# Optimization experiments

Measured on AMD Instinct MI355X. Metric: run time of the kernel, lower is better.

Reference implementation:

```python
import jax, jax.numpy as jnp
import numpy as np

B, N, F, H = 2, 2048, 1024, 16
HD = F // H
SQRT_D = float(np.sqrt(F))  # note: module scales by sqrt(in_c), not sqrt(head_dim)


def setup_inputs() -> dict:
    key = jax.random.key(0)
    ks = jax.random.split(key, 9)
    s = 1.0 / np.sqrt(F)
    mk = lambda k: jax.random.uniform(k, (F, F), jnp.float32, -s, s)
    mb = lambda k: jax.random.uniform(k, (F,), jnp.float32, -s, s)
    return {
        "x": jax.random.normal(ks[0], (B, N, F), jnp.float32),
        "Wq": mk(ks[1]), "bq": mb(ks[2]),
        "Wk": mk(ks[3]), "bk": mb(ks[4]),
        "Wv": mk(ks[5]), "bv": mb(ks[6]),
        "Wo": mk(ks[7]), "bo": mb(ks[8]),
    }


def reference(x, Wq, bq, Wk, bk, Wv, bv, Wo, bo):
    b, n, f = x.shape
    # projections (torch Linear: x @ W.T + b); view to (b, n, h, hd)
    q = (x @ Wq.T + bq).reshape(b, n, H, HD)
    k = (x @ Wk.T + bk).reshape(b, n, H, HD)
    v = (x @ Wv.T + bv).reshape(b, n, H, HD)
    score = jnp.einsum('bihd,bjhd->bhij', q, k)
    attn = jax.nn.softmax(score / SQRT_D, axis=-1)
    o = jnp.einsum('bhij,bjhd->bihd', attn, v).reshape(b, n, f)
    return o @ Wo.T + bo
```

## Files before the change

### kernel.cpp

```cpp
#include <hip/hip_runtime.h>
#include <hip/hip_bf16.h>
#include <stdint.h>
#include <stddef.h>

typedef __bf16 bf16;
typedef __attribute__((ext_vector_type(8))) __bf16 bf16x8;
typedef __attribute__((ext_vector_type(4))) __bf16 bf16x4;
typedef __attribute__((ext_vector_type(2))) __bf16 bf16x2;
typedef __attribute__((ext_vector_type(4))) float f32x4;

#define MFMA16(a, b, c) __builtin_amdgcn_mfma_f32_16x16x32_bf16(a, b, c, 0, 0, 0)

#define BB 2
#define SEQ 2048
#define FDIM 1024
#define NH 16
#define HD 64
#define M_TOK 4096
#define N_QKV 3072

#define CSC 0.04508422f

__device__ __forceinline__ void gll16(const bf16* g, bf16* l) {
    __builtin_amdgcn_global_load_lds(
        (const __attribute__((address_space(1))) void*)g,
        (__attribute__((address_space(3))) void*)l, 16, 0, 0);
}

__device__ __forceinline__ bf16 pack_bf16(float f) {
    uint32_t u = __builtin_bit_cast(uint32_t, f);
    uint16_t h = (uint16_t)((u + 0x8000u) >> 16);
    return __builtin_bit_cast(bf16, h);
}

__device__ __forceinline__ uint32_t pk2(float a, float b) {
#if __has_builtin(__builtin_amdgcn_cvt_pk_bf16_f32)
    bf16x2 t = __builtin_amdgcn_cvt_pk_bf16_f32(a, b);
    return __builtin_bit_cast(uint32_t, t);
#else
    uint32_t ua = __builtin_bit_cast(uint32_t, a) + 0x8000u;
    uint32_t ub = __builtin_bit_cast(uint32_t, b) + 0x8000u;
    return __builtin_amdgcn_perm(ub, ua, 0x07060302);
#endif
}

__global__ __launch_bounds__(256) void convert_k(
    const float* __restrict__ x,
    const float* __restrict__ Wq, const float* __restrict__ bq,
    const float* __restrict__ Wk, const float* __restrict__ bk,
    const float* __restrict__ Wv, const float* __restrict__ bv,
    const float* __restrict__ Wo,
    bf16* __restrict__ xb, bf16* __restrict__ Wcat, bf16* __restrict__ Wob,
    float* __restrict__ bcat)
{
    const int tid = blockIdx.x * blockDim.x + threadIdx.x;
    const int nt = gridDim.x * blockDim.x;
    const int NX4 = M_TOK * FDIM / 4;
    const int NW4 = FDIM * FDIM / 4;

    for (int i = tid; i < NX4; i += nt) {
        float4 v = ((const float4*)x)[i];
        bf16x4 o; o[0] = (bf16)v.x; o[1] = (bf16)v.y; o[2] = (bf16)v.z; o[3] = (bf16)v.w;
        ((bf16x4*)xb)[i] = o;
    }
    for (int i = tid; i < NW4; i += nt) {
        float4 v = ((const float4*)Wq)[i];
        bf16x4 o;
        o[0] = (bf16)(v.x * CSC); o[1] = (bf16)(v.y * CSC);
        o[2] = (bf16)(v.z * CSC); o[3] = (bf16)(v.w * CSC);
        ((bf16x4*)Wcat)[i] = o;
        v = ((const float4*)Wk)[i];
        o[0] = (bf16)v.x; o[1] = (bf16)v.y; o[2] = (bf16)v.z; o[3] = (bf16)v.w;
        ((bf16x4*)Wcat)[NW4 + i] = o;
        v = ((const float4*)Wv)[i];
        o[0] = (bf16)v.x; o[1] = (bf16)v.y; o[2] = (bf16)v.z; o[3] = (bf16)v.w;
        ((bf16x4*)Wcat)[2 * NW4 + i] = o;
        v = ((const float4*)Wo)[i];
        o[0] = (bf16)v.x; o[1] = (bf16)v.y; o[2] = (bf16)v.z; o[3] = (bf16)v.w;
        ((bf16x4*)Wob)[i] = o;
    }
    for (int i = tid; i < FDIM; i += nt) {
        bcat[i] = bq[i] * CSC;
        bcat[FDIM + i] = bk[i];
        bcat[2 * FDIM + i] = bv[i];
    }
}

template<int MT>
__global__ __launch_bounds__(256) void gemm_bt(
    const bf16* __restrict__ A,
    const bf16* __restrict__ Bw,
    const float* __restrict__ bias,
    bf16* __restrict__ Cb,
    float* __restrict__ Cf,
    bf16* __restrict__ VtOut,
    int M, int N, int K)
{
    constexpr int RI = MT / 32;
    __shared__ __align__(16) bf16 As[2][MT * 32];
    __shared__ __align__(16) bf16 Bs[2][128 * 32];

    const int tid = threadIdx.x;
    const int lane = tid & 63;
    const int wave = tid >> 6;
    const int m0 = blockIdx.y * MT;
    const int n0 = blockIdx.x * 128;
    const int wm = (wave >> 1) * (MT / 2);
    const int wn = (wave & 1) * 64;
    const int lrow = lane & 15;
    const int lk8 = (lane >> 4) * 8;

    f32x4 acc[RI][4] = {};

    const int srow = wave * 16 + (lane >> 2);
    const int scol = (lane & 3) * 8;
    const bf16* Ag = A + (size_t)(m0 + srow) * K + scol;
    const bf16* Bg = Bw + (size_t)(n0 + srow) * K + scol;
    const int wo = (wave * 16) * 32;

    gll16(Ag, &As[0][wo]);
    if (MT == 128) gll16(Ag + (size_t)64 * K, &As[0][wo + 2048]);
    gll16(Bg, &Bs[0][wo]);
    gll16(Bg + (size_t)64 * K, &Bs[0][wo + 2048]);

    for (int k0 = 0, it = 0; k0 < K; k0 += 32, ++it) {
        const int cur = it & 1;
        __syncthreads();

        if (k0 + 32 < K) {
            const int nxt = cur ^ 1;
            gll16(Ag + k0 + 32, &As[nxt][wo]);
            if (MT == 128) gll16(Ag + (size_t)64 * K + k0 + 32, &As[nxt][wo + 2048]);
            gll16(Bg + k0 + 32, &Bs[nxt][wo]);
            gll16(Bg + (size_t)64 * K + k0 + 32, &Bs[nxt][wo + 2048]);
        }

        bf16x8 af[RI], bfr[4];
#pragma unroll
        for (int s = 0; s < RI; ++s)
            af[s] = *(const bf16x8*)&As[cur][(wm + s * 16 + lrow) * 32 + lk8];
#pragma unroll
        for (int s = 0; s < 4; ++s)
            bfr[s] = *(const bf16x8*)&Bs[cur][(wn + s * 16 + lrow) * 32 + lk8];
#pragma unroll
        for (int i = 0; i < RI; ++i)
#pragma unroll
            for (int j = 0; j < 4; ++j)
                acc[i][j] = MFMA16(af[i], bfr[j], acc[i][j]);
    }

    const int r0 = (lane >> 4) * 4;
    if (MT == 128 && VtOut && n0 >= 2048) {
        const int bql = (m0 >> 11);
#pragma unroll
        for (int i = 0; i < RI; ++i) {
#pragma unroll
            for (int j = 0; j < 4; ++j) {
                const int col = n0 + wn + j * 16 + lrow;
                const float bsv = bias[col];
                const int vh = col - 2048;
                const int row = m0 + wm + i * 16 + r0;
                const int jj = row & (SEQ - 1);
                const int g = jj & 63;
                const int jj2 = (jj & ~63) | ((g >> 5) << 5)
                              | (((g >> 2) & 3) << 3) | (((g >> 4) & 1) << 2);
                bf16x4 vv;
#pragma unroll
                for (int r = 0; r < 4; ++r)
                    vv[r] = pack_bf16(acc[i][j][r] + bsv);
                *(bf16x4*)&VtOut[((size_t)bql * 16 * 64 + vh) * SEQ + jj2] = vv;
            }
        }
        return;
    }
#pragma unroll
    for (int i = 0; i < RI; ++i) {
#pragma unroll
        for (int j = 0; j < 4; ++j) {
            const int col = n0 + wn + j * 16 + lrow;
            const float bsv = bias[col];
#pragma unroll
            for (int r = 0; r < 4; ++r) {
                const int row = m0 + wm + i * 16 + r0 + r;
                const float v = acc[i][j][r] + bsv;
                if (Cb) Cb[(size_t)row * N + col] = pack_bf16(v);
                else    Cf[(size_t)row * N + col] = v;
            }
        }
    }
}

__global__ __launch_bounds__(512, 4) void attn_k(
    const bf16* __restrict__ QKV,
    const bf16* __restrict__ Vt,
    bf16* __restrict__ O)
{
    const int bx = blockIdx.x;
    const int bh = (bx & 7) + 8 * ((bx >> 3) & 3);
    const int qblk = bx >> 5;
    const int b = bh >> 4;
    const int h = bh & 15;
    const int lane = threadIdx.x & 63;
    const int wave = threadIdx.x >> 6;
    const int qg = wave & 3;
    const int jp = wave >> 2;
    const int lrow = lane & 15;
    const int quad = lane >> 4;
    const int lk8 = quad * 8;

    __shared__ __align__(16) bf16 Ks[2][2][128 * 32];
    __shared__ __align__(16) bf16 Vs[2][4][64 * 32];

    const size_t base = (size_t)b * SEQ * N_QKV;
    const bf16* Qp = QKV + base + h * HD;
    const bf16* Kp = QKV + base + FDIM + h * HD;
    const bf16* Vtp = Vt + (size_t)bh * HD * SEQ;

    const int qr0 = qblk * 128 + qg * 32;

    bf16x8 qf[2][2];
#pragma unroll
    for (int qt = 0; qt < 2; ++qt)
#pragma unroll
        for (int ks = 0; ks < 2; ++ks)
            qf[qt][ks] = *(const bf16x8*)(Qp + (size_t)(qr0 + qt * 16 + lrow) * N_QKV
                                          + ks * 32 + lk8);

    bf16x8 ones8;
#pragma unroll
    for (int e = 0; e < 8; ++e) ones8[e] = (bf16)1.0f;

    const f32x4 zf = {0.f, 0.f, 0.f, 0.f};

    f32x4 o[2][4] = {};
    f32x4 o4[2] = {};

    const int srow = wave * 16 + (lane >> 2);
    const int scol = (lane & 3) * 8;
    const bf16* kg = Kp + (size_t)srow * N_QKV + scol;
    const int vsrow = qg * 16 + (lane >> 2);
    const bf16* vg = Vtp + (size_t)vsrow * SEQ + jp * 32 + scol;
    const int kwo = wave * 512;

    gll16(kg,      &Ks[0][0][0] + kwo);
    gll16(kg + 32, &Ks[0][1][0] + kwo);
    gll16(vg,      &Vs[0][0][0] + kwo);
    gll16(vg + 64, &Vs[0][2][0] + kwo);
    kg += (size_t)128 * N_QKV;
    vg += 128;

    for (int jt = 0; jt < SEQ / 128; ++jt) {
        const int cur = jt & 1;
        __syncthreads();

        if (jt + 1 < SEQ / 128) {
            const int nxt = cur ^ 1;
            gll16(kg,      &Ks[nxt][0][0] + kwo);
            gll16(kg + 32, &Ks[nxt][1][0] + kwo);
            gll16(vg,      &Vs[nxt][0][0] + kwo);
            gll16(vg + 64, &Vs[nxt][2][0] + kwo);
            kg += (size_t)128 * N_QKV;
            vg += 128;
        }

#pragma unroll
        for (int pp = 0; pp < 2; ++pp) {
            const int p = (pp << 1) | jp;
            f32x4 Sp[2][2];
            __builtin_amdgcn_s_setprio(1);
#pragma unroll
            for (int m = 0; m < 2; ++m) {
                const int jn = 2 * p + m;
                bf16x8 kb0 = *(const bf16x8*)&Ks[cur][0][(jn * 16 + lrow) * 32 + lk8];
                bf16x8 kb1 = *(const bf16x8*)&Ks[cur][1][(jn * 16 + lrow) * 32 + lk8];
                Sp[m][0] = MFMA16(kb0, qf[0][0], zf);
                Sp[m][0] = MFMA16(kb1, qf[0][1], Sp[m][0]);
                Sp[m][1] = MFMA16(kb0, qf[1][0], zf);
                Sp[m][1] = MFMA16(kb1, qf[1][1], Sp[m][1]);
            }
            __builtin_amdgcn_s_setprio(0);

            union { bf16x8 v; uint32_t d[4]; } pb[2];
#pragma unroll
            for (int qt = 0; qt < 2; ++qt) {
                const f32x4 s0 = Sp[0][qt];
                const f32x4 s1 = Sp[1][qt];
                pb[qt].d[0] = pk2(__builtin_amdgcn_exp2f(s0[0]),
                                  __builtin_amdgcn_exp2f(s0[1]));
                pb[qt].d[1] = pk2(__builtin_amdgcn_exp2f(s0[2]),
                                  __builtin_amdgcn_exp2f(s0[3]));
                pb[qt].d[2] = pk2(__builtin_amdgcn_exp2f(s1[0]),
                                  __builtin_amdgcn_exp2f(s1[1]));
                pb[qt].d[3] = pk2(__builtin_amdgcn_exp2f(s1[2]),
                                  __builtin_amdgcn_exp2f(s1[3]));
            }

            __builtin_amdgcn_s_setprio(1);
            o4[0] = MFMA16(ones8, pb[0].v, o4[0]);
            o4[1] = MFMA16(ones8, pb[1].v, o4[1]);
#pragma unroll
            for (int df = 0; df < 4; ++df) {
                bf16x8 vA = *(const bf16x8*)&Vs[cur][p][(df * 16 + lrow) * 32 + lk8];
                o[0][df] = MFMA16(vA, pb[0].v, o[0][df]);
                o[1][df] = MFMA16(vA, pb[1].v, o[1][df]);
            }
            __builtin_amdgcn_s_setprio(0);
        }
    }

    __syncthreads();
    float* shO = (float*)Ks;
    float* shS = (float*)Vs;
    if (jp == 1) {
#pragma unroll
        for (int qt = 0; qt < 2; ++qt)
#pragma unroll
            for (int df = 0; df < 4; ++df)
                *(f32x4*)&shO[((((qt * 4 + df) * 4) + qg) * 64 + lane) * 4] = o[qt][df];
        shS[(qg * 64 + lane) * 2 + 0] = o4[0][0];
        shS[(qg * 64 + lane) * 2 + 1] = o4[1][0];
    }
    __syncthreads();
    if (jp == 1) return;

#pragma unroll
    for (int qt = 0; qt < 2; ++qt)
#pragma unroll
        for (int df = 0; df < 4; ++df) {
            f32x4 t = *(const f32x4*)&shO[((((qt * 4 + df) * 4) + qg) * 64 + lane) * 4];
            o[qt][df][0] += t[0]; o[qt][df][1] += t[1];
            o[qt][df][2] += t[2]; o[qt][df][3] += t[3];
        }
    const float den0 = o4[0][0] + shS[(qg * 64 + lane) * 2 + 0];
    const float den1 = o4[1][0] + shS[(qg * 64 + lane) * 2 + 1];

#pragma unroll
    for (int qt = 0; qt < 2; ++qt) {
        const float inv = 1.0f / (qt ? den1 : den0);
        const int q = qr0 + qt * 16 + lrow;
#pragma unroll
        for (int df = 0; df < 4; ++df) {
            bf16x4 vv;
#pragma unroll
            for (int r = 0; r < 4; ++r)
                vv[r] = pack_bf16(o[qt][df][r] * inv);
            *(bf16x4*)&O[(size_t)(b * SEQ + q) * FDIM + h * HD + df * 16 + quad * 4] = vv;
        }
    }
}

extern "C" void kernel_launch(void* const* d_in, const int* in_sizes, int n_in,
                              void* d_out, int out_size, void* d_ws, size_t ws_size,
                              hipStream_t stream) {
    (void)in_sizes; (void)n_in; (void)out_size; (void)ws_size;
    const float* x  = (const float*)d_in[0];
    const float* Wq = (const float*)d_in[1];
    const float* bq = (const float*)d_in[2];
    const float* Wk = (const float*)d_in[3];
    const float* bk = (const float*)d_in[4];
    const float* Wv = (const float*)d_in[5];
    const float* bv = (const float*)d_in[6];
    const float* Wo = (const float*)d_in[7];
    const float* bo = (const float*)d_in[8];
    float* out = (float*)d_out;

    char* ws = (char*)d_ws;
    bf16* xb    = (bf16*)(ws);
    bf16* Wcat  = (bf16*)(ws + 8388608);
    bf16* Wob   = (bf16*)(ws + 14680064);
    float* bcat = (float*)(ws + 16777216);
    bf16* QKV   = (bf16*)(ws + 16789504);
    bf16* Vt    = (bf16*)(ws + 41955328);
    bf16* Ob    = xb;

    convert_k<<<dim3(1024), dim3(256), 0, stream>>>(x, Wq, bq, Wk, bk, Wv, bv, Wo,
                                                    xb, Wcat, Wob, bcat);
    gemm_bt<128><<<dim3(N_QKV / 128, M_TOK / 128), dim3(256), 0, stream>>>(
        xb, Wcat, bcat, QKV, nullptr, Vt, M_TOK, N_QKV, FDIM);
    attn_k<<<dim3((SEQ / 128) * BB * NH), dim3(512), 0, stream>>>(QKV, Vt, Ob);
    gemm_bt<64><<<dim3(FDIM / 128, M_TOK / 64), dim3(256), 0, stream>>>(
        Ob, Wob, bo, nullptr, out, nullptr, M_TOK, FDIM, FDIM);
}
```

Measured before the change: 186.1 us.

## Replace GEMM with 256x128 tile, 8-wave, triple-buffered swizzled-LDS kernel

The templated 128/64-row GEMM is replaced by a single kernel using 512 threads, 256x128 output tiles and a K-step of 64. A three-stage global_load_lds pipeline uses explicit vmcnt waits and barriers, with XOR-swizzled LDS rows to avoid bank conflicts and s_setprio around the MFMA bursts. The aim is more operand reuse per LDS byte and better overlap of loads with MFMA work. It needs 144 KB of dynamic LDS, so only one block fits per CU. The output projection then launches only 128 blocks, which may leave many CUs idle.

```diff
diff --git a/kernel.cpp b/kernel.cpp
--- a/kernel.cpp
+++ b/kernel.cpp
@@ -86,8 +86,7 @@
     }
 }
 
-template<int MT>
-__global__ __launch_bounds__(256) void gemm_bt(
+__global__ __launch_bounds__(512, 2) void gemm8(
     const bf16* __restrict__ A,
     const bf16* __restrict__ Bw,
     const float* __restrict__ bias,
@@ -96,70 +95,111 @@
     bf16* __restrict__ VtOut,
     int M, int N, int K)
 {
-    constexpr int RI = MT / 32;
-    __shared__ __align__(16) bf16 As[2][MT * 32];
-    __shared__ __align__(16) bf16 Bs[2][128 * 32];
-
+    extern __shared__ char smem[];
     const int tid = threadIdx.x;
     const int lane = tid & 63;
     const int wave = tid >> 6;
-    const int m0 = blockIdx.y * MT;
+    const int wr = wave >> 2;
+    const int wc = wave & 3;
+    const int m0 = blockIdx.y * 256;
     const int n0 = blockIdx.x * 128;
-    const int wm = (wave >> 1) * (MT / 2);
-    const int wn = (wave & 1) * 64;
     const int lrow = lane & 15;
-    const int lk8 = (lane >> 4) * 8;
-
-    f32x4 acc[RI][4] = {};
-
-    const int srow = wave * 16 + (lane >> 2);
-    const int scol = (lane & 3) * 8;
-    const bf16* Ag = A + (size_t)(m0 + srow) * K + scol;
-    const bf16* Bg = Bw + (size_t)(n0 + srow) * K + scol;
-    const int wo = (wave * 16) * 32;
-
-    gll16(Ag, &As[0][wo]);
-    if (MT == 128) gll16(Ag + (size_t)64 * K, &As[0][wo + 2048]);
-    gll16(Bg, &Bs[0][wo]);
-    gll16(Bg + (size_t)64 * K, &Bs[0][wo + 2048]);
-
-    for (int k0 = 0, it = 0; k0 < K; k0 += 32, ++it) {
-        const int cur = it & 1;
-        __syncthreads();
-
-        if (k0 + 32 < K) {
-            const int nxt = cur ^ 1;
-            gll16(Ag + k0 + 32, &As[nxt][wo]);
-            if (MT == 128) gll16(Ag + (size_t)64 * K + k0 + 32, &As[nxt][wo + 2048]);
-            gll16(Bg + k0 + 32, &Bs[nxt][wo]);
-            gll16(Bg + (size_t)64 * K + k0 + 32, &Bs[nxt][wo + 2048]);
-        }
-
-        bf16x8 af[RI], bfr[4];
-#pragma unroll
-        for (int s = 0; s < RI; ++s)
-            af[s] = *(const bf16x8*)&As[cur][(wm + s * 16 + lrow) * 32 + lk8];
-#pragma unroll
-        for (int s = 0; s < 4; ++s)
-            bfr[s] = *(const bf16x8*)&Bs[cur][(wn + s * 16 + lrow) * 32 + lk8];
-#pragma unroll
-        for (int i = 0; i < RI; ++i)
-#pragma unroll
-            for (int j = 0; j < 4; ++j)
-                acc[i][j] = MFMA16(af[i], bfr[j], acc[i][j]);
-    }
-
-    const int r0 = (lane >> 4) * 4;
-    if (MT == 128 && VtOut && n0 >= 2048) {
+    const int quad = lane >> 4;
+    const int NT = K >> 6;
+
+    const int strow = wave * 8 + (lane >> 3);
+    const int koff = (((lane & 7) ^ (lane >> 3)) << 3);
+    const bf16* agp = A + (size_t)(m0 + strow) * K + koff;
+    const bf16* bgp = Bw + (size_t)(n0 + strow) * K + koff;
+    const int swo = wave * 1024;
+
+    const int axrow = (wr * 128 + lrow) * 128;
+    const int bxrow = (wc * 32 + lrow) * 128;
+    const int soff0 = ((quad) ^ (lrow & 7)) * 16;
+    const int soff1 = ((4 + quad) ^ (lrow & 7)) * 16;
+
+    f32x4 acc[8][2] = {};
+
+#define STAGE_A(slot, kt, c) \
+    gll16(agp + (size_t)(c) * 64 * K + (size_t)(kt) * 64, \
+          (bf16*)(smem + (slot) * 49152 + (c) * 8192 + swo))
+#define STAGE_B(slot, kt, c) \
+    gll16(bgp + (size_t)(c) * 64 * K + (size_t)(kt) * 64, \
+          (bf16*)(smem + (slot) * 49152 + 32768 + (c) * 8192 + swo))
+
+    STAGE_A(0, 0, 0); STAGE_A(0, 0, 1); STAGE_A(0, 0, 2); STAGE_A(0, 0, 3);
+    STAGE_B(0, 0, 0); STAGE_B(0, 0, 1);
+    if (NT > 1) {
+        STAGE_A(1, 1, 0); STAGE_A(1, 1, 1); STAGE_A(1, 1, 2); STAGE_A(1, 1, 3);
+        STAGE_B(1, 1, 0); STAGE_B(1, 1, 1);
+    }
+    asm volatile("s_waitcnt vmcnt(6)" ::: "memory");
+    __builtin_amdgcn_s_barrier();
+
+    int cur = 0;
+    for (int t = 0; t < NT; ++t) {
+        const int s2 = (cur >= 1) ? cur - 1 : cur + 2;
+        const char* sA = smem + cur * 49152;
+        const char* sB = sA + 32768;
+        const bool pf = (t + 2 < NT);
+        bf16x8 bfr[2][2];
+
+#pragma unroll
+        for (int ph = 0; ph < 2; ++ph) {
+            bf16x8 af[4][2];
+            if (ph == 0) {
+#pragma unroll
+                for (int j = 0; j < 2; ++j) {
+                    bfr[j][0] = *(const bf16x8*)(sB + bxrow + j * 2048 + soff0);
+                    bfr[j][1] = *(const bf16x8*)(sB + bxrow + j * 2048 + soff1);
+                }
+            }
+#pragma unroll
+            for (int i2 = 0; i2 < 4; ++i2) {
+                af[i2][0] = *(const bf16x8*)(sA + axrow + (ph * 4 + i2) * 2048 + soff0);
+                af[i2][1] = *(const bf16x8*)(sA + axrow + (ph * 4 + i2) * 2048 + soff1);
+            }
+            if (pf) {
+                if (ph == 0) {
+                    STAGE_A(s2, t + 2, 0); STAGE_A(s2, t + 2, 1); STAGE_A(s2, t + 2, 2);
+                } else {
+                    STAGE_A(s2, t + 2, 3); STAGE_B(s2, t + 2, 0); STAGE_B(s2, t + 2, 1);
+                }
+            }
+            __builtin_amdgcn_s_barrier();
+            asm volatile("s_waitcnt lgkmcnt(0)" ::: "memory");
+            __builtin_amdgcn_sched_barrier(0);
+            __builtin_amdgcn_s_setprio(1);
+#pragma unroll
+            for (int i2 = 0; i2 < 4; ++i2)
+#pragma unroll
+                for (int j = 0; j < 2; ++j) {
+                    acc[ph * 4 + i2][j] = MFMA16(af[i2][0], bfr[j][0], acc[ph * 4 + i2][j]);
+                    acc[ph * 4 + i2][j] = MFMA16(af[i2][1], bfr[j][1], acc[ph * 4 + i2][j]);
+                }
+            __builtin_amdgcn_s_setprio(0);
+            if (ph == 1) {
+                if (pf) asm volatile("s_waitcnt vmcnt(6)" ::: "memory");
+                else    asm volatile("s_waitcnt vmcnt(0)" ::: "memory");
+            }
+            __builtin_amdgcn_s_barrier();
+        }
+        cur = (cur + 1 == 3) ? 0 : cur + 1;
+    }
+#undef STAGE_A
+#undef STAGE_B
+
+    const int r0 = quad * 4;
+    if (VtOut && n0 >= 2048) {
         const int bql = (m0 >> 11);
 #pragma unroll
-        for (int i = 0; i < RI; ++i) {
-#pragma unroll
-            for (int j = 0; j < 4; ++j) {
-                const int col = n0 + wn + j * 16 + lrow;
+        for (int i = 0; i < 8; ++i) {
+#pragma unroll
+            for (int j = 0; j < 2; ++j) {
+                const int col = n0 + wc * 32 + j * 16 + lrow;
                 const float bsv = bias[col];
                 const int vh = col - 2048;
-                const int row = m0 + wm + i * 16 + r0;
+                const int row = m0 + wr * 128 + i * 16 + r0;
                 const int jj = row & (SEQ - 1);
                 const int g = jj & 63;
                 const int jj2 = (jj & ~63) | ((g >> 5) << 5)
@@ -174,14 +214,14 @@
         return;
     }
 #pragma unroll
-    for (int i = 0; i < RI; ++i) {
-#pragma unroll
-        for (int j = 0; j < 4; ++j) {
-            const int col = n0 + wn + j * 16 + lrow;
+    for (int i = 0; i < 8; ++i) {
+#pragma unroll
+        for (int j = 0; j < 2; ++j) {
+            const int col = n0 + wc * 32 + j * 16 + lrow;
             const float bsv = bias[col];
 #pragma unroll
             for (int r = 0; r < 4; ++r) {
-                const int row = m0 + wm + i * 16 + r0 + r;
+                const int row = m0 + wr * 128 + i * 16 + r0 + r;
                 const float v = acc[i][j][r] + bsv;
                 if (Cb) Cb[(size_t)row * N + col] = pack_bf16(v);
                 else    Cf[(size_t)row * N + col] = v;
@@ -373,11 +413,19 @@
     bf16* Vt    = (bf16*)(ws + 41955328);
     bf16* Ob    = xb;
 
+    static bool s_attr_done = false;
+    if (!s_attr_done) {
+        (void)hipFuncSetAttribute(reinterpret_cast<const void*>(gemm8),
+                                  hipFuncAttributeMaxDynamicSharedMemorySize,
+                                  147456);
+        s_attr_done = true;
+    }
+
     convert_k<<<dim3(1024), dim3(256), 0, stream>>>(x, Wq, bq, Wk, bk, Wv, bv, Wo,
                                                     xb, Wcat, Wob, bcat);
-    gemm_bt<128><<<dim3(N_QKV / 128, M_TOK / 128), dim3(256), 0, stream>>>(
+    gemm8<<<dim3(N_QKV / 128, M_TOK / 256), dim3(512), 147456, stream>>>(
         xb, Wcat, bcat, QKV, nullptr, Vt, M_TOK, N_QKV, FDIM);
     attn_k<<<dim3((SEQ / 128) * BB * NH), dim3(512), 0, stream>>>(QKV, Vt, Ob);
-    gemm_bt<64><<<dim3(FDIM / 128, M_TOK / 64), dim3(256), 0, stream>>>(
+    gemm8<<<dim3(FDIM / 128, M_TOK / 256), dim3(512), 147456, stream>>>(
         Ob, Wob, bo, nullptr, out, nullptr, M_TOK, FDIM, FDIM);
 }
```

Result: slower. 191.5 us (+2.9%).

## Replace QKV projection GEMM with 256x256-tile 8-wave swizzled pipelined kernel

Applied to the files above, without the earlier changes.

Adds a new gemm256 kernel for the fused QKV projection. It uses 256x256 output tiles, 512 threads, 128 KB of dynamic LDS double buffering with an XOR swizzle, and prefetch of the next K-tile split into four phases, each followed by a vmcnt wait and barrier. The aim is more data reuse per block and less LDS bank conflict and load latency than the 128x128 gemm_bt. The trade-off is only 12x16=192 blocks on the device, which may underfill the CUs, plus higher register and LDS use. The V-transpose epilogue moves into the new kernel, and gemm_bt is simplified to the fp32-only output path.

```diff
diff --git a/kernel.cpp b/kernel.cpp
--- a/kernel.cpp
+++ b/kernel.cpp
@@ -86,14 +86,151 @@
     }
 }
 
+__global__ __launch_bounds__(512, 2) void gemm256(
+    const bf16* __restrict__ A,
+    const bf16* __restrict__ Bw,
+    const float* __restrict__ bias,
+    bf16* __restrict__ Cb,
+    bf16* __restrict__ VtOut,
+    int M, int N, int K)
+{
+    extern __shared__ char smem[];
+    const int tid = threadIdx.x;
+    const int lane = tid & 63;
+    const int wave = tid >> 6;
+    const int wr = wave >> 2;
+    const int wc = wave & 3;
+    const int m0 = blockIdx.y * 256;
+    const int n0 = blockIdx.x * 256;
+    const int lrow = lane & 15;
+    const int quad = lane >> 4;
+    const int NT = K >> 6;
+
+    const int l8 = lane >> 3;
+    const int kx = ((lane & 7) ^ l8) << 3;
+    const int lcl = wave * 16 + l8;
+
+#define ASTG(sl, kt, mh, c) do { \
+    const int _lc = lcl + (c) * 8; \
+    const int _gr = m0 + ((_lc >> 6) << 7) + ((mh) << 6) + (_lc & 63); \
+    gll16(A + (size_t)_gr * K + (size_t)(kt) * 64 + kx, \
+          (bf16*)(smem + (sl) * 65536 + (mh) * 16384 + wave * 2048 + (c) * 1024)); \
+} while (0)
+#define BSTG(sl, kt, nh, c) do { \
+    const int _lc = lcl + (c) * 8; \
+    const int _gc = n0 + ((_lc >> 5) << 6) + ((nh) << 5) + (_lc & 31); \
+    gll16(Bw + (size_t)_gc * K + (size_t)(kt) * 64 + kx, \
+          (bf16*)(smem + (sl) * 65536 + 32768 + (nh) * 16384 + wave * 2048 + (c) * 1024)); \
+} while (0)
+
+    const int swz0 = ((quad ^ (lrow & 7)) << 4);
+    const int swz1 = (((4 + quad) ^ (lrow & 7)) << 4);
+    const int arow = (wr * 64 + lrow) * 128;
+    const int brow = (wc * 32 + lrow) * 128;
+
+    f32x4 acc[8][4] = {};
+    bf16x8 af[4][2];
+    bf16x8 bc[2][2][2];
+
+    ASTG(0, 0, 0, 0); ASTG(0, 0, 0, 1);
+    BSTG(0, 0, 0, 0); BSTG(0, 0, 0, 1);
+    BSTG(0, 0, 1, 0); BSTG(0, 0, 1, 1);
+    ASTG(0, 0, 1, 0); ASTG(0, 0, 1, 1);
+    asm volatile("s_waitcnt vmcnt(4)" ::: "memory");
+    __builtin_amdgcn_s_barrier();
+
+    for (int t = 0; t < NT; ++t) {
+        const int sl = t & 1;
+        const int ns = sl ^ 1;
+        const char* sb = smem + sl * 65536;
+        const bool pf = (t + 1 < NT);
+
+#pragma unroll
+        for (int ph = 0; ph < 4; ++ph) {
+            const int mh = ph >> 1, nh = ph & 1;
+            if (pf) {
+                if (ph == 0)      { ASTG(ns, t + 1, 0, 0); ASTG(ns, t + 1, 0, 1); }
+                else if (ph == 1) { BSTG(ns, t + 1, 0, 0); BSTG(ns, t + 1, 0, 1); }
+                else if (ph == 2) { BSTG(ns, t + 1, 1, 0); BSTG(ns, t + 1, 1, 1); }
+                else              { ASTG(ns, t + 1, 1, 0); ASTG(ns, t + 1, 1, 1); }
+            }
+            if (nh == 0) {
+#pragma unroll
+                for (int iq = 0; iq < 4; ++iq) {
+                    af[iq][0] = *(const bf16x8*)(sb + mh * 16384 + arow + iq * 2048 + swz0);
+                    af[iq][1] = *(const bf16x8*)(sb + mh * 16384 + arow + iq * 2048 + swz1);
+                }
+            }
+            if (ph == 0 || ph == 1) {
+#pragma unroll
+                for (int jq = 0; jq < 2; ++jq) {
+                    bc[nh][jq][0] = *(const bf16x8*)(sb + 32768 + nh * 16384 + brow + jq * 2048 + swz0);
+                    bc[nh][jq][1] = *(const bf16x8*)(sb + 32768 + nh * 16384 + brow + jq * 2048 + swz1);
+                }
+            }
+            __builtin_amdgcn_s_setprio(1);
+#pragma unroll
+            for (int iq = 0; iq < 4; ++iq)
+#pragma unroll
+                for (int jq = 0; jq < 2; ++jq) {
+                    acc[mh * 4 + iq][nh * 2 + jq] =
+                        MFMA16(af[iq][0], bc[nh][jq][0], acc[mh * 4 + iq][nh * 2 + jq]);
+                    acc[mh * 4 + iq][nh * 2 + jq] =
+                        MFMA16(af[iq][1], bc[nh][jq][1], acc[mh * 4 + iq][nh * 2 + jq]);
+                }
+            __builtin_amdgcn_s_setprio(0);
+            if (pf) asm volatile("s_waitcnt vmcnt(4)" ::: "memory");
+            else    asm volatile("s_waitcnt vmcnt(0)" ::: "memory");
+            __builtin_amdgcn_s_barrier();
+        }
+    }
+#undef ASTG
+#undef BSTG
+
+    if (VtOut && n0 >= 2048) {
+        const int bql = (m0 >> 11);
+#pragma unroll
+        for (int i = 0; i < 8; ++i) {
+#pragma unroll
+            for (int j = 0; j < 4; ++j) {
+                const int col = n0 + wc * 64 + (j >> 1) * 32 + (j & 1) * 16 + lrow;
+                const float bsv = bias[col];
+                const int vh = col - 2048;
+                const int row = m0 + wr * 128 + (i >> 2) * 64 + (i & 3) * 16 + quad * 4;
+                const int jj = row & (SEQ - 1);
+                const int g = jj & 63;
+                const int jj2 = (jj & ~63) | ((g >> 5) << 5)
+                              | (((g >> 2) & 3) << 3) | (((g >> 4) & 1) << 2);
+                bf16x4 vv;
+#pragma unroll
+                for (int r = 0; r < 4; ++r)
+                    vv[r] = pack_bf16(acc[i][j][r] + bsv);
+                *(bf16x4*)&VtOut[((size_t)bql * 16 * 64 + vh) * SEQ + jj2] = vv;
+            }
+        }
+        return;
+    }
+#pragma unroll
+    for (int i = 0; i < 8; ++i) {
+#pragma unroll
+        for (int j = 0; j < 4; ++j) {
+            const int col = n0 + wc * 64 + (j >> 1) * 32 + (j & 1) * 16 + lrow;
+            const float bsv = bias[col];
+#pragma unroll
+            for (int r = 0; r < 4; ++r) {
+                const int row = m0 + wr * 128 + (i >> 2) * 64 + (i & 3) * 16 + quad * 4 + r;
+                Cb[(size_t)row * N + col] = pack_bf16(acc[i][j][r] + bsv);
+            }
+        }
+    }
+}
+
 template<int MT>
 __global__ __launch_bounds__(256) void gemm_bt(
     const bf16* __restrict__ A,
     const bf16* __restrict__ Bw,
     const float* __restrict__ bias,
-    bf16* __restrict__ Cb,
     float* __restrict__ Cf,
-    bf16* __restrict__ VtOut,
     int M, int N, int K)
 {
     constexpr int RI = MT / 32;
@@ -150,29 +287,6 @@
     }
 
     const int r0 = (lane >> 4) * 4;
-    if (MT == 128 && VtOut && n0 >= 2048) {
-        const int bql = (m0 >> 11);
-#pragma unroll
-        for (int i = 0; i < RI; ++i) {
-#pragma unroll
-            for (int j = 0; j < 4; ++j) {
-                const int col = n0 + wn + j * 16 + lrow;
-                const float bsv = bias[col];
-                const int vh = col - 2048;
-                const int row = m0 + wm + i * 16 + r0;
-                const int jj = row & (SEQ - 1);
-                const int g = jj & 63;
-                const int jj2 = (jj & ~63) | ((g >> 5) << 5)
-                              | (((g >> 2) & 3) << 3) | (((g >> 4) & 1) << 2);
-                bf16x4 vv;
-#pragma unroll
-                for (int r = 0; r < 4; ++r)
-                    vv[r] = pack_bf16(acc[i][j][r] + bsv);
-                *(bf16x4*)&VtOut[((size_t)bql * 16 * 64 + vh) * SEQ + jj2] = vv;
-            }
-        }
-        return;
-    }
 #pragma unroll
     for (int i = 0; i < RI; ++i) {
 #pragma unroll
@@ -182,9 +296,7 @@
 #pragma unroll
             for (int r = 0; r < 4; ++r) {
                 const int row = m0 + wm + i * 16 + r0 + r;
-                const float v = acc[i][j][r] + bsv;
-                if (Cb) Cb[(size_t)row * N + col] = pack_bf16(v);
-                else    Cf[(size_t)row * N + col] = v;
+                Cf[(size_t)row * N + col] = acc[i][j][r] + bsv;
             }
         }
     }
@@ -373,11 +485,19 @@
     bf16* Vt    = (bf16*)(ws + 41955328);
     bf16* Ob    = xb;
 
+    static bool s_attr_done = false;
+    if (!s_attr_done) {
+        (void)hipFuncSetAttribute(reinterpret_cast<const void*>(gemm256),
+                                  hipFuncAttributeMaxDynamicSharedMemorySize,
+                                  131072);
+        s_attr_done = true;
+    }
+
     convert_k<<<dim3(1024), dim3(256), 0, stream>>>(x, Wq, bq, Wk, bk, Wv, bv, Wo,
                                                     xb, Wcat, Wob, bcat);
-    gemm_bt<128><<<dim3(N_QKV / 128, M_TOK / 128), dim3(256), 0, stream>>>(
-        xb, Wcat, bcat, QKV, nullptr, Vt, M_TOK, N_QKV, FDIM);
+    gemm256<<<dim3(N_QKV / 256, M_TOK / 256), dim3(512), 131072, stream>>>(
+        xb, Wcat, bcat, QKV, Vt, M_TOK, N_QKV, FDIM);
     attn_k<<<dim3((SEQ / 128) * BB * NH), dim3(512), 0, stream>>>(QKV, Vt, Ob);
     gemm_bt<64><<<dim3(FDIM / 128, M_TOK / 64), dim3(256), 0, stream>>>(
-        Ob, Wob, bo, nullptr, out, nullptr, M_TOK, FDIM, FDIM);
-}
+        Ob, Wob, bo, out, M_TOK, FDIM, FDIM);
+}
```

Result: no change. 183.3 us (-1.5%).
